# Optimization experiments

Measured on AMD Instinct MI355X. Metric: run time of the kernel, lower is better.

Reference implementation:

```python
import jax, jax.numpy as jnp
import numpy as np

N = 100000
E = 3200000
B = 8192
IN_DIM = 18   # enc_dim for khops=2
HID = 64
EMB = 32


def setup_inputs() -> dict:
    key = jax.random.key(0)
    ks = jax.random.split(key, 10)
    x = jax.random.normal(ks[0], (N, IN_DIM), dtype=jnp.float32)
    ei = jax.random.randint(ks[1], (2, E), 0, N, dtype=jnp.int64)
    targets = jax.random.randint(ks[2], (2, B), 0, N, dtype=jnp.int64)
    # GCN layer params (glorot-ish scale)
    W1 = jax.random.normal(ks[3], (IN_DIM, HID), dtype=jnp.float32) / np.sqrt(IN_DIM)
    b1 = jnp.zeros((HID,), dtype=jnp.float32)
    W2 = jax.random.normal(ks[4], (HID, EMB), dtype=jnp.float32) / np.sqrt(HID)
    b2 = jnp.zeros((EMB,), dtype=jnp.float32)
    Wo = jax.random.normal(ks[5], (EMB, 1), dtype=jnp.float32) / np.sqrt(EMB)
    bo = jnp.zeros((1,), dtype=jnp.float32)
    return {"x": x, "ei": ei, "targets": targets,
            "W1": W1, "b1": b1, "W2": W2, "b2": b2, "Wo": Wo, "bo": bo}


def _gcn_conv(x, W, b, src, dst, norm, n_nodes):
    # x' = D^{-1/2}(A+I)D^{-1/2} X W + b  (self-loops already in src/dst)
    h = x @ W                                  # [N, F_out]
    msg = h[src] * norm[:, None]               # [E+N, F_out] gather
    agg = jax.ops.segment_sum(msg, dst, num_segments=n_nodes)  # scatter-add
    return agg + b


def reference(x, ei, targets, W1, b1, W2, b2, Wo, bo):
    n = x.shape[0]
    loop = jnp.arange(n, dtype=ei.dtype)
    src = jnp.concatenate([ei[0], loop])
    dst = jnp.concatenate([ei[1], loop])
    deg = jax.ops.segment_sum(jnp.ones_like(src, dtype=x.dtype), dst, num_segments=n)
    dis = jax.lax.rsqrt(deg)                   # deg >= 1 (self-loops)
    norm = dis[src] * dis[dst]
    # 2-layer GCN (khops=2): relu between layers, dropout=0 (eval)
    h = jax.nn.relu(_gcn_conv(x, W1, b1, src, dst, norm, n))
    z = _gcn_conv(h, W2, b2, src, dst, norm, n)
    # node-pair multiply + linear head
    pair = z[targets[0]] * z[targets[1]]       # [B, EMB]
    return pair @ Wo + bo                      # [B, 1]
```

## Files before the change

kernel.cpp:

```cpp
#include <hip/hip_runtime.h>

#define IN_DIM 18
#define XPAD 20
#define HID 64
#define EMB 32
#define NGROUP 8
#define PSHIFT 9
#define PMAX 200
#define BCAP 80
#define TILE 4096
#define SCAP 16896
#define NPB 16

typedef int vint4 __attribute__((ext_vector_type(4)));
typedef unsigned int u32;

__device__ inline float4 shfl_f4(float4 v, int srcLane) {
    float4 r;
    r.x = __shfl(v.x, srcLane);
    r.y = __shfl(v.y, srcLane);
    r.z = __shfl(v.z, srcLane);
    r.w = __shfl(v.w, srcLane);
    return r;
}

__device__ inline float4 shfl_xor_f4(float4 v, int m) {
    v.x = __shfl_xor(v.x, m);
    v.y = __shfl_xor(v.y, m);
    v.z = __shfl_xor(v.z, m);
    v.w = __shfl_xor(v.w, m);
    return v;
}


__global__ void k_init(int* __restrict__ deg, int* __restrict__ gcnt, int n) {
    int i = blockIdx.x * 256 + threadIdx.x;
    if (i < n) deg[i] = 1;
    if (i < 256) gcnt[i] = 0;
}


__global__ void k_part(const int* __restrict__ src, const int* __restrict__ dst,
                       int* __restrict__ gcnt, u32* __restrict__ gbuf,
                       int e, int Pp, int cap) {
    __shared__ u32 sbuf[PMAX][BCAP];
    __shared__ int scnt[PMAX];
    __shared__ int sbase[PMAX];
    int tid = threadIdx.x;
    int ntile = (e + TILE - 1) / TILE;
    for (int tile = blockIdx.x; tile < ntile; tile += gridDim.x) {
        for (int p = tid; p < Pp; p += 256) scnt[p] = 0;
        __syncthreads();
#pragma unroll
        for (int r = 0; r < TILE / 1024; ++r) {
            int i = tile * TILE + (r * 256 + tid) * 4;
            if (i + 4 <= e) {
                vint4 s4 = __builtin_nontemporal_load((const vint4*)(src + i));
                vint4 d4 = __builtin_nontemporal_load((const vint4*)(dst + i));
#pragma unroll
                for (int k = 0; k < 4; ++k) {
                    int d = d4[k];
                    int p = d >> PSHIFT;
                    u32 pr = ((u32)s4[k] << PSHIFT) | (u32)(d & 511);
                    int pos = atomicAdd(&scnt[p], 1);
                    if (pos < BCAP) sbuf[p][pos] = pr;
                    else {
                        int gp = atomicAdd(&gcnt[p], 1);
                        __builtin_nontemporal_store(pr, &gbuf[(size_t)p * cap + gp]);
                    }
                }
            } else if (i < e) {
                for (int k = i; k < e; ++k) {
                    int d = dst[k];
                    int p = d >> PSHIFT;
                    u32 pr = ((u32)src[k] << PSHIFT) | (u32)(d & 511);
                    int pos = atomicAdd(&scnt[p], 1);
                    if (pos < BCAP) sbuf[p][pos] = pr;
                    else {
                        int gp = atomicAdd(&gcnt[p], 1);
                        __builtin_nontemporal_store(pr, &gbuf[(size_t)p * cap + gp]);
                    }
                }
            }
        }
        __syncthreads();
        for (int p = tid; p < Pp; p += 256)
            sbase[p] = atomicAdd(&gcnt[p], min(scnt[p], BCAP));
        __syncthreads();
        int wid = tid >> 6, lane = tid & 63;
        for (int p = wid; p < Pp; p += 4) {
            int c = min(scnt[p], BCAP);
            int b = sbase[p];
            for (int k = lane; k < c; k += 64)
                __builtin_nontemporal_store(sbuf[p][k], &gbuf[(size_t)p * cap + b + k]);
        }
        __syncthreads();
    }
}


__global__ void k_gscan(const int* __restrict__ gcnt, int* __restrict__ gbase, int Pp) {
    __shared__ int s[256];
    int t = threadIdx.x;
    int v = (t < Pp) ? gcnt[t] : 0;
    s[t] = v;
    __syncthreads();
    for (int off = 1; off < 256; off <<= 1) {
        int u = (t >= off) ? s[t - off] : 0;
        __syncthreads();
        s[t] += u;
        __syncthreads();
    }
    if (t < Pp) gbase[t] = s[t] - v;
}


__global__ void k_build(const u32* __restrict__ gbuf, const int* __restrict__ gcnt,
                        const int* __restrict__ gbase, int* __restrict__ deg,
                        float* __restrict__ dis, int* __restrict__ row_ptr,
                        int* __restrict__ adj, int cap, int n) {
    __shared__ u32 spairs[SCAP];
    __shared__ int sdeg[512];
    __shared__ int sexcl[512];
    __shared__ int swp[512];
    __shared__ int sscan[512];
    int p = blockIdx.x;
    int tid = threadIdx.x;
    int lo = p << PSHIFT;
    int nn = min(n - lo, 512);
    int cnt = gcnt[p];
    int base = gbase[p];
    const u32* buf = gbuf + (size_t)p * cap;

    sdeg[tid] = 0;
    int scap = min(cnt, SCAP);
    for (int k = tid; k < scap; k += 512)
        spairs[k] = __builtin_nontemporal_load(&buf[k]);
    __syncthreads();
    for (int k = tid; k < cnt; k += 512) {
        u32 pr = (k < SCAP) ? spairs[k] : __builtin_nontemporal_load(&buf[k]);
        atomicAdd(&sdeg[pr & 511], 1);
    }
    __syncthreads();
    int v = sdeg[tid];
    sscan[tid] = v;
    __syncthreads();
    for (int off = 1; off < 512; off <<= 1) {
        int u = (tid >= off) ? sscan[tid - off] : 0;
        __syncthreads();
        sscan[tid] += u;
        __syncthreads();
    }
    sexcl[tid] = sscan[tid] - v;
    swp[tid] = 0;
    __syncthreads();
    if (tid < nn) {
        int dg = sdeg[tid] + 1;
        deg[lo + tid] = dg;
        dis[lo + tid] = rsqrtf((float)dg);
        row_ptr[lo + tid] = base + sexcl[tid];
    }
    for (int k = tid; k < cnt; k += 512) {
        u32 pr = (k < SCAP) ? spairs[k] : __builtin_nontemporal_load(&buf[k]);
        int dl = pr & 511;
        int slot = sexcl[dl] + atomicAdd(&swp[dl], 1);
        adj[base + slot] = (int)(pr >> PSHIFT);
    }
}


__global__ void k_count_part(const int* __restrict__ dst, int* __restrict__ deg,
                             int e, int nrange, int n) {
    int g  = blockIdx.x & (NGROUP - 1);
    int lo = g * nrange;
    int hi = min(n, lo + nrange);
    int bid  = blockIdx.x >> 3;
    int nblk = gridDim.x >> 3;
    int i0   = (bid * 256 + threadIdx.x) * 4;
    int step = nblk * 256 * 4;
    for (int i = i0; i < e; i += step) {
        if (i + 4 <= e) {
            int4 d4 = *(const int4*)(dst + i);
            if (d4.x >= lo && d4.x < hi) atomicAdd(&deg[d4.x], 1);
            if (d4.y >= lo && d4.y < hi) atomicAdd(&deg[d4.y], 1);
            if (d4.z >= lo && d4.z < hi) atomicAdd(&deg[d4.z], 1);
            if (d4.w >= lo && d4.w < hi) atomicAdd(&deg[d4.w], 1);
        } else {
            for (int k = i; k < e; ++k) {
                int d = dst[k];
                if (d >= lo && d < hi) atomicAdd(&deg[d], 1);
            }
        }
    }
}

__global__ void k_dis(const int* __restrict__ deg, float* __restrict__ dis, int n) {
    int i = blockIdx.x * 256 + threadIdx.x;
    if (i < n) dis[i] = rsqrtf((float)deg[i]);
}

__global__ void k_scanA(const int* __restrict__ deg, int* __restrict__ row_ptr,
                        int* __restrict__ blksums, int n) {
    __shared__ int s[1024];
    int tid = threadIdx.x;
    int i = blockIdx.x * 1024 + tid;
    int v = (i < n) ? (deg[i] - 1) : 0;
    s[tid] = v;
    __syncthreads();
    for (int off = 1; off < 1024; off <<= 1) {
        int t = (tid >= off) ? s[tid - off] : 0;
        __syncthreads();
        s[tid] += t;
        __syncthreads();
    }
    if (i < n) row_ptr[i] = s[tid] - v;
    if (tid == 1023) blksums[blockIdx.x] = s[1023];
}

__global__ void k_scanB(const int* __restrict__ blksums, int* __restrict__ blkoffs, int nb) {
    __shared__ int s[1024];
    int tid = threadIdx.x;
    int v = (tid < nb) ? blksums[tid] : 0;
    s[tid] = v;
    __syncthreads();
    for (int off = 1; off < 1024; off <<= 1) {
        int t = (tid >= off) ? s[tid - off] : 0;
        __syncthreads();
        s[tid] += t;
        __syncthreads();
    }
    if (tid < nb) blkoffs[tid] = s[tid] - v;
}

__global__ void k_scanC(int* __restrict__ row_ptr, const int* __restrict__ blkoffs,
                        int* __restrict__ write_ptr, int n) {
    int i = blockIdx.x * 1024 + threadIdx.x;
    if (i < n) {
        int r = row_ptr[i] + blkoffs[blockIdx.x];
        row_ptr[i] = r;
        write_ptr[i] = r;
    }
}

__global__ void k_fill_part(const int* __restrict__ src, const int* __restrict__ dst,
                            int* __restrict__ write_ptr, int* __restrict__ adj,
                            int e, int nrange, int n) {
    int g  = blockIdx.x & (NGROUP - 1);
    int lo = g * nrange;
    int hi = min(n, lo + nrange);
    int bid  = blockIdx.x >> 3;
    int nblk = gridDim.x >> 3;
    int i0   = (bid * 256 + threadIdx.x) * 4;
    int step = nblk * 256 * 4;
    for (int i = i0; i < e; i += step) {
        if (i + 4 <= e) {
            int4 d4 = *(const int4*)(dst + i);
            if (d4.x >= lo && d4.x < hi) { int slot = atomicAdd(&write_ptr[d4.x], 1); adj[slot] = src[i];     }
            if (d4.y >= lo && d4.y < hi) { int slot = atomicAdd(&write_ptr[d4.y], 1); adj[slot] = src[i + 1]; }
            if (d4.z >= lo && d4.z < hi) { int slot = atomicAdd(&write_ptr[d4.z], 1); adj[slot] = src[i + 2]; }
            if (d4.w >= lo && d4.w < hi) { int slot = atomicAdd(&write_ptr[d4.w], 1); adj[slot] = src[i + 3]; }
        } else {
            for (int k = i; k < e; ++k) {
                int d = dst[k];
                if (d >= lo && d < hi) { int slot = atomicAdd(&write_ptr[d], 1); adj[slot] = src[k]; }
            }
        }
    }
}


__global__ void k_xn(const float* __restrict__ x, const float* __restrict__ dis,
                     float* __restrict__ xn, int n) {
    int gid = blockIdx.x * 256 + threadIdx.x;
    if (gid >= n * 5) return;
    int i = gid / 5, s = gid - (gid / 5) * 5;
    float dn = dis[i];
    const float* xr = x + (size_t)i * IN_DIM;
    float4 v;
    int k = s * 4;
    v.x = (k + 0 < IN_DIM) ? xr[k + 0] * dn : 0.f;
    v.y = (k + 1 < IN_DIM) ? xr[k + 1] * dn : 0.f;
    v.z = (k + 2 < IN_DIM) ? xr[k + 2] * dn : 0.f;
    v.w = (k + 3 < IN_DIM) ? xr[k + 3] * dn : 0.f;
    *(float4*)(xn + (size_t)i * XPAD + k) = v;
}


__global__ void k_agg1f(const float* __restrict__ xn, const int* __restrict__ row_ptr,
                        const int* __restrict__ deg, const int* __restrict__ adj,
                        const float* __restrict__ dis, const float* __restrict__ W1,
                        const float* __restrict__ b1, const float* __restrict__ W2,
                        float* __restrict__ hn2, int n) {
    __shared__ float sw[IN_DIM * HID];
    __shared__ float sw2[HID * EMB];
    __shared__ float sb[HID];
    __shared__ __align__(16) float sagg[4][XPAD];
    __shared__ float sh[4][HID];
    int tid = threadIdx.x;
    for (int t = tid; t < IN_DIM * HID; t += 256) sw[t] = W1[t];
    for (int t = tid; t < HID * EMB; t += 256) sw2[t] = W2[t];
    if (tid < HID) sb[tid] = b1[tid];
    __syncthreads();
    int lane = tid & 63;
    int wv = tid >> 6;
    int eg = lane / 5;
    int sl = lane - eg * 5;
    bool act = eg < 12;

    for (int nd = wv; nd < NPB; nd += 4) {
        int node = blockIdx.x * NPB + nd;
        if (node >= n) break;
        int beg = row_ptr[node];
        int cnt = deg[node] - 1;
        const int* a = adj + beg;
        float4 acc = make_float4(0.f, 0.f, 0.f, 0.f);
        int base = 0;
        for (; base + 24 <= cnt; base += 24) {
            if (act) {
                int j0 = a[base + eg];
                int j1 = a[base + 12 + eg];
                float4 v0 = *(const float4*)(xn + (size_t)j0 * XPAD + sl * 4);
                float4 v1 = *(const float4*)(xn + (size_t)j1 * XPAD + sl * 4);
                acc.x += v0.x + v1.x; acc.y += v0.y + v1.y;
                acc.z += v0.z + v1.z; acc.w += v0.w + v1.w;
            }
        }
        if (act && base + eg < cnt) {
            float4 v = *(const float4*)(xn + (size_t)a[base + eg] * XPAD + sl * 4);
            acc.x += v.x; acc.y += v.y; acc.z += v.z; acc.w += v.w;
        }
        if (act && base + 12 + eg < cnt) {
            float4 v = *(const float4*)(xn + (size_t)a[base + 12 + eg] * XPAD + sl * 4);
            acc.x += v.x; acc.y += v.y; acc.z += v.z; acc.w += v.w;
        }
        float4 t = shfl_f4(acc, lane + 30);
        if (lane < 30) { acc.x += t.x; acc.y += t.y; acc.z += t.z; acc.w += t.w; }
        t = shfl_f4(acc, lane + 15);
        if (lane < 15) { acc.x += t.x; acc.y += t.y; acc.z += t.z; acc.w += t.w; }
        t = shfl_f4(acc, lane + 10);
        if (lane < 5) { acc.x += t.x; acc.y += t.y; acc.z += t.z; acc.w += t.w; }
        t = shfl_f4(acc, lane + 5);
        if (lane < 5) { acc.x += t.x; acc.y += t.y; acc.z += t.z; acc.w += t.w; }
        float dn = dis[node];
        if (lane < 5) {
            float4 s4v = *(const float4*)(xn + (size_t)node * XPAD + lane * 4);
            acc.x += s4v.x; acc.y += s4v.y; acc.z += s4v.z; acc.w += s4v.w;
            *(float4*)&sagg[wv][lane * 4] = acc;
        }
        float s = 0.f;
#pragma unroll
        for (int k = 0; k < IN_DIM; ++k) s += sagg[wv][k] * sw[k * HID + lane];
        float hv = dn * s + sb[lane];
        sh[wv][lane] = hv > 0.f ? hv : 0.f;
        int g = lane & 31, half = lane >> 5;
        float s2 = 0.f;
#pragma unroll
        for (int k = 0; k < 32; ++k)
            s2 += sh[wv][half * 32 + k] * sw2[(half * 32 + k) * EMB + g];
        s2 += __shfl_xor(s2, 32);
        if (half == 0) hn2[(size_t)node * EMB + g] = dn * s2;
    }
}


__global__ void k_agg2(const float* __restrict__ hn2, const int* __restrict__ row_ptr,
                       const int* __restrict__ deg, const int* __restrict__ adj,
                       const float* __restrict__ dis, const float* __restrict__ b2,
                       float* __restrict__ z, int n) {
    int node = blockIdx.x * 4 + (threadIdx.x >> 6);
    if (node >= n) return;
    int lane = threadIdx.x & 63;
    int eg = lane >> 3;
    int d4 = lane & 7;
    int beg = row_ptr[node];
    int cnt = deg[node] - 1;
    const int* a = adj + beg;
    float4 acc = make_float4(0.f, 0.f, 0.f, 0.f);
    int base = 0;
    for (; base + 24 <= cnt; base += 24) {
        int j0 = a[base + eg];
        int j1 = a[base + 8 + eg];
        int j2 = a[base + 16 + eg];
        float4 v0 = *(const float4*)(hn2 + (size_t)j0 * EMB + d4 * 4);
        float4 v1 = *(const float4*)(hn2 + (size_t)j1 * EMB + d4 * 4);
        float4 v2 = *(const float4*)(hn2 + (size_t)j2 * EMB + d4 * 4);
        acc.x += v0.x + v1.x + v2.x; acc.y += v0.y + v1.y + v2.y;
        acc.z += v0.z + v1.z + v2.z; acc.w += v0.w + v1.w + v2.w;
    }
    int kk = base + eg;
    if (kk < cnt) {
        float4 v = *(const float4*)(hn2 + (size_t)a[kk] * EMB + d4 * 4);
        acc.x += v.x; acc.y += v.y; acc.z += v.z; acc.w += v.w;
    }
    kk += 8;
    if (kk < cnt) {
        float4 v = *(const float4*)(hn2 + (size_t)a[kk] * EMB + d4 * 4);
        acc.x += v.x; acc.y += v.y; acc.z += v.z; acc.w += v.w;
    }
    kk += 8;
    if (kk < cnt) {
        float4 v = *(const float4*)(hn2 + (size_t)a[kk] * EMB + d4 * 4);
        acc.x += v.x; acc.y += v.y; acc.z += v.z; acc.w += v.w;
    }
    float4 t = shfl_xor_f4(acc, 8);
    acc.x += t.x; acc.y += t.y; acc.z += t.z; acc.w += t.w;
    t = shfl_xor_f4(acc, 16);
    acc.x += t.x; acc.y += t.y; acc.z += t.z; acc.w += t.w;
    t = shfl_xor_f4(acc, 32);
    acc.x += t.x; acc.y += t.y; acc.z += t.z; acc.w += t.w;
    if (eg == 0) {
        float4 self = *(const float4*)(hn2 + (size_t)node * EMB + d4 * 4);
        float4 bb = *(const float4*)(b2 + d4 * 4);
        float dn = dis[node];
        float4 o;
        o.x = dn * (acc.x + self.x) + bb.x;
        o.y = dn * (acc.y + self.y) + bb.y;
        o.z = dn * (acc.z + self.z) + bb.z;
        o.w = dn * (acc.w + self.w) + bb.w;
        *(float4*)(z + (size_t)node * EMB + d4 * 4) = o;
    }
}


__global__ void k_head(const float* __restrict__ z, const int* __restrict__ tg,
                       const float* __restrict__ Wo, const float* __restrict__ bo,
                       float* __restrict__ out, int btot) {
    int i = blockIdx.x * 256 + threadIdx.x;
    if (i >= btot) return;
    int t0 = tg[i], t1 = tg[btot + i];
    const float* z0 = z + (size_t)t0 * EMB;
    const float* z1 = z + (size_t)t1 * EMB;
    float acc = 0.f;
#pragma unroll
    for (int g = 0; g < EMB; ++g) acc += z0[g] * z1[g] * Wo[g];
    out[i] = acc + bo[0];
}


extern "C" void kernel_launch(void* const* d_in, const int* in_sizes, int n_in,
                              void* d_out, int out_size, void* d_ws, size_t ws_size,
                              hipStream_t stream) {
    const float* x  = (const float*)d_in[0];
    const int*   ei = (const int*)d_in[1];
    const int*   tg = (const int*)d_in[2];
    const float* W1 = (const float*)d_in[3];
    const float* b1 = (const float*)d_in[4];
    const float* W2 = (const float*)d_in[5];
    const float* b2 = (const float*)d_in[6];
    const float* Wo = (const float*)d_in[7];
    const float* bo = (const float*)d_in[8];
    float* out = (float*)d_out;

    int n = in_sizes[0] / IN_DIM;
    int e = in_sizes[1] / 2;
    int b = in_sizes[2] / 2;
    const int* src = ei;
    const int* dst = ei + e;

    char* ws = (char*)d_ws;
    size_t off = 0;
    auto alloc = [&](size_t bytes) -> char* {
        char* p = ws + off;
        off += (bytes + 255) & ~(size_t)255;
        return p;
    };
    int*   deg       = (int*)alloc((size_t)n * 4);
    int*   row_ptr   = (int*)alloc((size_t)n * 4);
    int*   write_ptr = (int*)alloc((size_t)n * 4);
    int*   blksums   = (int*)alloc(1024 * 4);
    int*   blkoffs   = (int*)alloc(1024 * 4);
    float* dis       = (float*)alloc((size_t)n * 4);
    int*   adj       = (int*)alloc((size_t)e * 4);
    float* xn        = (float*)alloc((size_t)n * XPAD * 4);
    float* bufA      = (float*)alloc((size_t)n * EMB * 4);
    float* bufB      = (float*)alloc((size_t)n * EMB * 4);
    int*   gcnt      = (int*)alloc(1024);
    int*   gbase     = (int*)alloc(1024);

    int Pp = (n + 511) >> PSHIFT;
    int meanb = (Pp > 0) ? (e / Pp) : e;
    int cap = meanb + meanb / 16 + 1024;
    size_t bucket_bytes = (size_t)Pp * cap * 4;
    bool use_buckets = (Pp <= PMAX) && (n < (1 << 23)) &&
                       ((off + bucket_bytes + 256) <= ws_size);
    u32* gbuf = (u32*)alloc(bucket_bytes);

    int nb1024 = (n + 1023) / 1024;
    int nrange = (n + NGROUP - 1) / NGROUP;

    k_init<<<(n + 255) / 256, 256, 0, stream>>>(deg, gcnt, n);

    if (use_buckets) {
        k_part<<<512, 256, 0, stream>>>(src, dst, gcnt, gbuf, e, Pp, cap);
        k_gscan<<<1, 256, 0, stream>>>(gcnt, gbase, Pp);
        k_build<<<Pp, 512, 0, stream>>>(gbuf, gcnt, gbase, deg, dis, row_ptr, adj, cap, n);
    } else {
        k_count_part<<<2048, 256, 0, stream>>>(dst, deg, e, nrange, n);
        k_dis<<<(n + 255) / 256, 256, 0, stream>>>(deg, dis, n);
        k_scanA<<<nb1024, 1024, 0, stream>>>(deg, row_ptr, blksums, n);
        k_scanB<<<1, 1024, 0, stream>>>(blksums, blkoffs, nb1024);
        k_scanC<<<nb1024, 1024, 0, stream>>>(row_ptr, blkoffs, write_ptr, n);
        k_fill_part<<<2048, 256, 0, stream>>>(src, dst, write_ptr, adj, e, nrange, n);
    }

    k_xn<<<((size_t)n * 5 + 255) / 256, 256, 0, stream>>>(x, dis, xn, n);
    k_agg1f<<<(n + NPB - 1) / NPB, 256, 0, stream>>>(xn, row_ptr, deg, adj, dis, W1, b1, W2, bufA, n);
    k_agg2<<<(n + 3) / 4, 256, 0, stream>>>(bufA, row_ptr, deg, adj, dis, b2, bufB, n);

    k_head<<<(b + 255) / 256, 256, 0, stream>>>(bufB, tg, Wo, bo, out, b);
}
```

Measured before the change: 233.3 us.

## Split layer-1 feature gather into column slices with separate SpMM passes

The padded 20-float normalized input rows are split into three column-sliced arrays (8, 8 and 4 floats), and the first-layer neighbor aggregation runs as three separate SpMM kernels, each gathering a narrow slice with full-wave lane use. Each slice's working set is smaller and more cache-resident, and lanes are no longer idle under the old 12x5 mapping. The dense W1/ReLU/W2 transform moves to its own kernel that reads the aggregated rows. The cost is reading the adjacency list three times, extra kernel launches, and a round trip of the aggregate through global memory.

```diff
diff --git a/kernel.cpp b/kernel.cpp
--- a/kernel.cpp
+++ b/kernel.cpp
@@ -14,15 +14,6 @@
 
 typedef int vint4 __attribute__((ext_vector_type(4)));
 typedef unsigned int u32;
-
-__device__ inline float4 shfl_f4(float4 v, int srcLane) {
-    float4 r;
-    r.x = __shfl(v.x, srcLane);
-    r.y = __shfl(v.y, srcLane);
-    r.z = __shfl(v.z, srcLane);
-    r.w = __shfl(v.w, srcLane);
-    return r;
-}
 
 __device__ inline float4 shfl_xor_f4(float4 v, int m) {
     v.x = __shfl_xor(v.x, m);
@@ -270,7 +261,8 @@
 
 
 __global__ void k_xn(const float* __restrict__ x, const float* __restrict__ dis,
-                     float* __restrict__ xn, int n) {
+                     float* __restrict__ xs0, float* __restrict__ xs1,
+                     float* __restrict__ xs2, int n) {
     int gid = blockIdx.x * 256 + threadIdx.x;
     if (gid >= n * 5) return;
     int i = gid / 5, s = gid - (gid / 5) * 5;
@@ -282,15 +274,105 @@
     v.y = (k + 1 < IN_DIM) ? xr[k + 1] * dn : 0.f;
     v.z = (k + 2 < IN_DIM) ? xr[k + 2] * dn : 0.f;
     v.w = (k + 3 < IN_DIM) ? xr[k + 3] * dn : 0.f;
-    *(float4*)(xn + (size_t)i * XPAD + k) = v;
-}
-
-
-__global__ void k_agg1f(const float* __restrict__ xn, const int* __restrict__ row_ptr,
-                        const int* __restrict__ deg, const int* __restrict__ adj,
-                        const float* __restrict__ dis, const float* __restrict__ W1,
-                        const float* __restrict__ b1, const float* __restrict__ W2,
-                        float* __restrict__ hn2, int n) {
+    if (s < 2)      *(float4*)(xs0 + (size_t)i * 8 + s * 4) = v;
+    else if (s < 4) *(float4*)(xs1 + (size_t)i * 8 + (s - 2) * 4) = v;
+    else            *(float4*)(xs2 + (size_t)i * 4) = v;
+}
+
+
+__global__ void k_sp2s(const float* __restrict__ xs, const int* __restrict__ row_ptr,
+                       const int* __restrict__ deg, const int* __restrict__ adj,
+                       float* __restrict__ agg, int aggoff, int n) {
+    int node = blockIdx.x * 4 + (threadIdx.x >> 6);
+    if (node >= n) return;
+    int lane = threadIdx.x & 63;
+    int eg = lane >> 1, sl = lane & 1;
+    int beg = row_ptr[node];
+    int cnt = deg[node] - 1;
+    const int* a = adj + beg;
+    float4 acc = make_float4(0.f, 0.f, 0.f, 0.f);
+    int base = 0;
+    for (; base + 64 <= cnt; base += 64) {
+        int j0 = __builtin_nontemporal_load(&a[base + eg]);
+        int j1 = __builtin_nontemporal_load(&a[base + 32 + eg]);
+        float4 v0 = *(const float4*)(xs + (size_t)j0 * 8 + sl * 4);
+        float4 v1 = *(const float4*)(xs + (size_t)j1 * 8 + sl * 4);
+        acc.x += v0.x + v1.x; acc.y += v0.y + v1.y;
+        acc.z += v0.z + v1.z; acc.w += v0.w + v1.w;
+    }
+    if (base + eg < cnt) {
+        int j = __builtin_nontemporal_load(&a[base + eg]);
+        float4 v = *(const float4*)(xs + (size_t)j * 8 + sl * 4);
+        acc.x += v.x; acc.y += v.y; acc.z += v.z; acc.w += v.w;
+    }
+    if (base + 32 + eg < cnt) {
+        int j = __builtin_nontemporal_load(&a[base + 32 + eg]);
+        float4 v = *(const float4*)(xs + (size_t)j * 8 + sl * 4);
+        acc.x += v.x; acc.y += v.y; acc.z += v.z; acc.w += v.w;
+    }
+    float4 t = shfl_xor_f4(acc, 2);  acc.x += t.x; acc.y += t.y; acc.z += t.z; acc.w += t.w;
+    t = shfl_xor_f4(acc, 4);  acc.x += t.x; acc.y += t.y; acc.z += t.z; acc.w += t.w;
+    t = shfl_xor_f4(acc, 8);  acc.x += t.x; acc.y += t.y; acc.z += t.z; acc.w += t.w;
+    t = shfl_xor_f4(acc, 16); acc.x += t.x; acc.y += t.y; acc.z += t.z; acc.w += t.w;
+    t = shfl_xor_f4(acc, 32); acc.x += t.x; acc.y += t.y; acc.z += t.z; acc.w += t.w;
+    if (lane < 2) {
+        float4 self = *(const float4*)(xs + (size_t)node * 8 + lane * 4);
+        acc.x += self.x; acc.y += self.y; acc.z += self.z; acc.w += self.w;
+        __builtin_nontemporal_store(acc.x, agg + (size_t)node * XPAD + aggoff + lane * 4 + 0);
+        __builtin_nontemporal_store(acc.y, agg + (size_t)node * XPAD + aggoff + lane * 4 + 1);
+        __builtin_nontemporal_store(acc.z, agg + (size_t)node * XPAD + aggoff + lane * 4 + 2);
+        __builtin_nontemporal_store(acc.w, agg + (size_t)node * XPAD + aggoff + lane * 4 + 3);
+    }
+}
+
+
+__global__ void k_sp1s(const float* __restrict__ xs, const int* __restrict__ row_ptr,
+                       const int* __restrict__ deg, const int* __restrict__ adj,
+                       float* __restrict__ agg, int aggoff, int n) {
+    int node = blockIdx.x * 4 + (threadIdx.x >> 6);
+    if (node >= n) return;
+    int lane = threadIdx.x & 63;
+    int beg = row_ptr[node];
+    int cnt = deg[node] - 1;
+    const int* a = adj + beg;
+    float4 acc = make_float4(0.f, 0.f, 0.f, 0.f);
+    int base = 0;
+    for (; base + 128 <= cnt; base += 128) {
+        int j0 = __builtin_nontemporal_load(&a[base + lane]);
+        int j1 = __builtin_nontemporal_load(&a[base + 64 + lane]);
+        float4 v0 = *(const float4*)(xs + (size_t)j0 * 4);
+        float4 v1 = *(const float4*)(xs + (size_t)j1 * 4);
+        acc.x += v0.x + v1.x; acc.y += v0.y + v1.y;
+        acc.z += v0.z + v1.z; acc.w += v0.w + v1.w;
+    }
+    if (base + lane < cnt) {
+        int j = __builtin_nontemporal_load(&a[base + lane]);
+        float4 v = *(const float4*)(xs + (size_t)j * 4);
+        acc.x += v.x; acc.y += v.y; acc.z += v.z; acc.w += v.w;
+    }
+    if (base + 64 + lane < cnt) {
+        int j = __builtin_nontemporal_load(&a[base + 64 + lane]);
+        float4 v = *(const float4*)(xs + (size_t)j * 4);
+        acc.x += v.x; acc.y += v.y; acc.z += v.z; acc.w += v.w;
+    }
+    for (int m = 1; m <= 32; m <<= 1) {
+        float4 t = shfl_xor_f4(acc, m);
+        acc.x += t.x; acc.y += t.y; acc.z += t.z; acc.w += t.w;
+    }
+    if (lane == 0) {
+        float4 self = *(const float4*)(xs + (size_t)node * 4);
+        acc.x += self.x; acc.y += self.y; acc.z += self.z; acc.w += self.w;
+        __builtin_nontemporal_store(acc.x, agg + (size_t)node * XPAD + aggoff + 0);
+        __builtin_nontemporal_store(acc.y, agg + (size_t)node * XPAD + aggoff + 1);
+        __builtin_nontemporal_store(acc.z, agg + (size_t)node * XPAD + aggoff + 2);
+        __builtin_nontemporal_store(acc.w, agg + (size_t)node * XPAD + aggoff + 3);
+    }
+}
+
+
+__global__ void k_w12(const float* __restrict__ agg, const float* __restrict__ dis,
+                      const float* __restrict__ W1, const float* __restrict__ b1,
+                      const float* __restrict__ W2, float* __restrict__ hn2, int n) {
     __shared__ float sw[IN_DIM * HID];
     __shared__ float sw2[HID * EMB];
     __shared__ float sb[HID];
@@ -303,49 +385,13 @@
     __syncthreads();
     int lane = tid & 63;
     int wv = tid >> 6;
-    int eg = lane / 5;
-    int sl = lane - eg * 5;
-    bool act = eg < 12;
-
     for (int nd = wv; nd < NPB; nd += 4) {
         int node = blockIdx.x * NPB + nd;
         if (node >= n) break;
-        int beg = row_ptr[node];
-        int cnt = deg[node] - 1;
-        const int* a = adj + beg;
-        float4 acc = make_float4(0.f, 0.f, 0.f, 0.f);
-        int base = 0;
-        for (; base + 24 <= cnt; base += 24) {
-            if (act) {
-                int j0 = a[base + eg];
-                int j1 = a[base + 12 + eg];
-                float4 v0 = *(const float4*)(xn + (size_t)j0 * XPAD + sl * 4);
-                float4 v1 = *(const float4*)(xn + (size_t)j1 * XPAD + sl * 4);
-                acc.x += v0.x + v1.x; acc.y += v0.y + v1.y;
-                acc.z += v0.z + v1.z; acc.w += v0.w + v1.w;
-            }
-        }
-        if (act && base + eg < cnt) {
-            float4 v = *(const float4*)(xn + (size_t)a[base + eg] * XPAD + sl * 4);
-            acc.x += v.x; acc.y += v.y; acc.z += v.z; acc.w += v.w;
-        }
-        if (act && base + 12 + eg < cnt) {
-            float4 v = *(const float4*)(xn + (size_t)a[base + 12 + eg] * XPAD + sl * 4);
-            acc.x += v.x; acc.y += v.y; acc.z += v.z; acc.w += v.w;
-        }
-        float4 t = shfl_f4(acc, lane + 30);
-        if (lane < 30) { acc.x += t.x; acc.y += t.y; acc.z += t.z; acc.w += t.w; }
-        t = shfl_f4(acc, lane + 15);
-        if (lane < 15) { acc.x += t.x; acc.y += t.y; acc.z += t.z; acc.w += t.w; }
-        t = shfl_f4(acc, lane + 10);
-        if (lane < 5) { acc.x += t.x; acc.y += t.y; acc.z += t.z; acc.w += t.w; }
-        t = shfl_f4(acc, lane + 5);
-        if (lane < 5) { acc.x += t.x; acc.y += t.y; acc.z += t.z; acc.w += t.w; }
         float dn = dis[node];
         if (lane < 5) {
-            float4 s4v = *(const float4*)(xn + (size_t)node * XPAD + lane * 4);
-            acc.x += s4v.x; acc.y += s4v.y; acc.z += s4v.z; acc.w += s4v.w;
-            *(float4*)&sagg[wv][lane * 4] = acc;
+            float4 v = *(const float4*)(agg + (size_t)node * XPAD + lane * 4);
+            *(float4*)&sagg[wv][lane * 4] = v;
         }
         float s = 0.f;
 #pragma unroll
@@ -471,7 +517,10 @@
     int*   blkoffs   = (int*)alloc(1024 * 4);
     float* dis       = (float*)alloc((size_t)n * 4);
     int*   adj       = (int*)alloc((size_t)e * 4);
-    float* xn        = (float*)alloc((size_t)n * XPAD * 4);
+    float* xs0       = (float*)alloc((size_t)n * 8 * 4);
+    float* xs1       = (float*)alloc((size_t)n * 8 * 4);
+    float* xs2       = (float*)alloc((size_t)n * 4 * 4);
+    float* agg       = (float*)alloc((size_t)n * XPAD * 4);
     float* bufA      = (float*)alloc((size_t)n * EMB * 4);
     float* bufB      = (float*)alloc((size_t)n * EMB * 4);
     int*   gcnt      = (int*)alloc(1024);
@@ -487,6 +536,7 @@
 
     int nb1024 = (n + 1023) / 1024;
     int nrange = (n + NGROUP - 1) / NGROUP;
+    int nblk4 = (n + 3) / 4;
 
     k_init<<<(n + 255) / 256, 256, 0, stream>>>(deg, gcnt, n);
 
@@ -503,9 +553,14 @@
         k_fill_part<<<2048, 256, 0, stream>>>(src, dst, write_ptr, adj, e, nrange, n);
     }
 
-    k_xn<<<((size_t)n * 5 + 255) / 256, 256, 0, stream>>>(x, dis, xn, n);
-    k_agg1f<<<(n + NPB - 1) / NPB, 256, 0, stream>>>(xn, row_ptr, deg, adj, dis, W1, b1, W2, bufA, n);
-    k_agg2<<<(n + 3) / 4, 256, 0, stream>>>(bufA, row_ptr, deg, adj, dis, b2, bufB, n);
+    k_xn<<<((size_t)n * 5 + 255) / 256, 256, 0, stream>>>(x, dis, xs0, xs1, xs2, n);
+
+    k_sp2s<<<nblk4, 256, 0, stream>>>(xs0, row_ptr, deg, adj, agg, 0, n);
+    k_sp2s<<<nblk4, 256, 0, stream>>>(xs1, row_ptr, deg, adj, agg, 8, n);
+    k_sp1s<<<nblk4, 256, 0, stream>>>(xs2, row_ptr, deg, adj, agg, 16, n);
+    k_w12<<<(n + NPB - 1) / NPB, 256, 0, stream>>>(agg, dis, W1, b1, W2, bufA, n);
+
+    k_agg2<<<nblk4, 256, 0, stream>>>(bufA, row_ptr, deg, adj, dis, b2, bufB, n);
 
     k_head<<<(b + 255) / 256, 256, 0, stream>>>(bufB, tg, Wo, bo, out, b);
 }
```

After: 299.1 us. 28.2% more time.

## Fold bucket scan into build, drop init launch, split layer-2 GEMM out of agg1

Applied to the files above, without the earlier changes.

Removes the separate global scan kernel by having each k_build block recompute the prefix over bucket counts in shared memory. In the bucket path, the full-size degree init kernel is replaced by a one-block zero of the counters. k_agg1f now handles one node per wave, with no W2 staged in shared memory, and writes the 64-wide hidden layer to a new buffer. A separate k_gemm2 kernel then applies W2. This should cut shared-memory use and raise occupancy in the aggregation kernel, and it removes small launches. In exchange it adds an extra round trip of the N×64 hidden tensor through global memory plus one more launch.

```diff
diff --git a/kernel.cpp b/kernel.cpp
--- a/kernel.cpp
+++ b/kernel.cpp
@@ -10,7 +10,6 @@
 #define BCAP 80
 #define TILE 4096
 #define SCAP 16896
-#define NPB 16
 
 typedef int vint4 __attribute__((ext_vector_type(4)));
 typedef unsigned int u32;
@@ -32,6 +31,10 @@
     return v;
 }
 
+
+__global__ void k_zero(int* __restrict__ gcnt) {
+    gcnt[threadIdx.x] = 0;
+}
 
 __global__ void k_init(int* __restrict__ deg, int* __restrict__ gcnt, int n) {
     int i = blockIdx.x * 256 + threadIdx.x;
@@ -99,26 +102,10 @@
 }
 
 
-__global__ void k_gscan(const int* __restrict__ gcnt, int* __restrict__ gbase, int Pp) {
-    __shared__ int s[256];
-    int t = threadIdx.x;
-    int v = (t < Pp) ? gcnt[t] : 0;
-    s[t] = v;
-    __syncthreads();
-    for (int off = 1; off < 256; off <<= 1) {
-        int u = (t >= off) ? s[t - off] : 0;
-        __syncthreads();
-        s[t] += u;
-        __syncthreads();
-    }
-    if (t < Pp) gbase[t] = s[t] - v;
-}
-
-
 __global__ void k_build(const u32* __restrict__ gbuf, const int* __restrict__ gcnt,
-                        const int* __restrict__ gbase, int* __restrict__ deg,
-                        float* __restrict__ dis, int* __restrict__ row_ptr,
-                        int* __restrict__ adj, int cap, int n) {
+                        int* __restrict__ deg, float* __restrict__ dis,
+                        int* __restrict__ row_ptr, int* __restrict__ adj,
+                        int cap, int n, int Pp) {
     __shared__ u32 spairs[SCAP];
     __shared__ int sdeg[512];
     __shared__ int sexcl[512];
@@ -129,8 +116,19 @@
     int lo = p << PSHIFT;
     int nn = min(n - lo, 512);
     int cnt = gcnt[p];
-    int base = gbase[p];
     const u32* buf = gbuf + (size_t)p * cap;
+
+    if (tid < 256) sscan[tid] = (tid < Pp) ? gcnt[tid] : 0;
+    __syncthreads();
+    for (int off = 1; off < 256; off <<= 1) {
+        int u = 0;
+        if (tid < 256 && tid >= off) u = sscan[tid - off];
+        __syncthreads();
+        if (tid < 256) sscan[tid] += u;
+        __syncthreads();
+    }
+    int base = sscan[p] - cnt;
+    __syncthreads();
 
     sdeg[tid] = 0;
     int scap = min(cnt, SCAP);
@@ -289,77 +287,78 @@
 __global__ void k_agg1f(const float* __restrict__ xn, const int* __restrict__ row_ptr,
                         const int* __restrict__ deg, const int* __restrict__ adj,
                         const float* __restrict__ dis, const float* __restrict__ W1,
-                        const float* __restrict__ b1, const float* __restrict__ W2,
-                        float* __restrict__ hn2, int n) {
+                        const float* __restrict__ b1, float* __restrict__ h, int n) {
     __shared__ float sw[IN_DIM * HID];
-    __shared__ float sw2[HID * EMB];
     __shared__ float sb[HID];
     __shared__ __align__(16) float sagg[4][XPAD];
-    __shared__ float sh[4][HID];
     int tid = threadIdx.x;
     for (int t = tid; t < IN_DIM * HID; t += 256) sw[t] = W1[t];
-    for (int t = tid; t < HID * EMB; t += 256) sw2[t] = W2[t];
     if (tid < HID) sb[tid] = b1[tid];
     __syncthreads();
+    int node = blockIdx.x * 4 + (tid >> 6);
+    if (node >= n) return;
     int lane = tid & 63;
     int wv = tid >> 6;
     int eg = lane / 5;
     int sl = lane - eg * 5;
     bool act = eg < 12;
-
-    for (int nd = wv; nd < NPB; nd += 4) {
-        int node = blockIdx.x * NPB + nd;
-        if (node >= n) break;
-        int beg = row_ptr[node];
-        int cnt = deg[node] - 1;
-        const int* a = adj + beg;
-        float4 acc = make_float4(0.f, 0.f, 0.f, 0.f);
-        int base = 0;
-        for (; base + 24 <= cnt; base += 24) {
-            if (act) {
-                int j0 = a[base + eg];
-                int j1 = a[base + 12 + eg];
-                float4 v0 = *(const float4*)(xn + (size_t)j0 * XPAD + sl * 4);
-                float4 v1 = *(const float4*)(xn + (size_t)j1 * XPAD + sl * 4);
-                acc.x += v0.x + v1.x; acc.y += v0.y + v1.y;
-                acc.z += v0.z + v1.z; acc.w += v0.w + v1.w;
-            }
+    int beg = row_ptr[node];
+    int cnt = deg[node] - 1;
+    const int* a = adj + beg;
+    float4 acc = make_float4(0.f, 0.f, 0.f, 0.f);
+    int base = 0;
+    for (; base + 24 <= cnt; base += 24) {
+        if (act) {
+            int j0 = a[base + eg];
+            int j1 = a[base + 12 + eg];
+            float4 v0 = *(const float4*)(xn + (size_t)j0 * XPAD + sl * 4);
+            float4 v1 = *(const float4*)(xn + (size_t)j1 * XPAD + sl * 4);
+            acc.x += v0.x + v1.x; acc.y += v0.y + v1.y;
+            acc.z += v0.z + v1.z; acc.w += v0.w + v1.w;
         }
-        if (act && base + eg < cnt) {
-            float4 v = *(const float4*)(xn + (size_t)a[base + eg] * XPAD + sl * 4);
-            acc.x += v.x; acc.y += v.y; acc.z += v.z; acc.w += v.w;
-        }
-        if (act && base + 12 + eg < cnt) {
-            float4 v = *(const float4*)(xn + (size_t)a[base + 12 + eg] * XPAD + sl * 4);
-            acc.x += v.x; acc.y += v.y; acc.z += v.z; acc.w += v.w;
-        }
-        float4 t = shfl_f4(acc, lane + 30);
-        if (lane < 30) { acc.x += t.x; acc.y += t.y; acc.z += t.z; acc.w += t.w; }
-        t = shfl_f4(acc, lane + 15);
-        if (lane < 15) { acc.x += t.x; acc.y += t.y; acc.z += t.z; acc.w += t.w; }
-        t = shfl_f4(acc, lane + 10);
-        if (lane < 5) { acc.x += t.x; acc.y += t.y; acc.z += t.z; acc.w += t.w; }
-        t = shfl_f4(acc, lane + 5);
-        if (lane < 5) { acc.x += t.x; acc.y += t.y; acc.z += t.z; acc.w += t.w; }
-        float dn = dis[node];
-        if (lane < 5) {
-            float4 s4v = *(const float4*)(xn + (size_t)node * XPAD + lane * 4);
-            acc.x += s4v.x; acc.y += s4v.y; acc.z += s4v.z; acc.w += s4v.w;
-            *(float4*)&sagg[wv][lane * 4] = acc;
-        }
-        float s = 0.f;
+    }
+    if (act && base + eg < cnt) {
+        float4 v = *(const float4*)(xn + (size_t)a[base + eg] * XPAD + sl * 4);
+        acc.x += v.x; acc.y += v.y; acc.z += v.z; acc.w += v.w;
+    }
+    if (act && base + 12 + eg < cnt) {
+        float4 v = *(const float4*)(xn + (size_t)a[base + 12 + eg] * XPAD + sl * 4);
+        acc.x += v.x; acc.y += v.y; acc.z += v.z; acc.w += v.w;
+    }
+    float4 t = shfl_f4(acc, lane + 30);
+    if (lane < 30) { acc.x += t.x; acc.y += t.y; acc.z += t.z; acc.w += t.w; }
+    t = shfl_f4(acc, lane + 15);
+    if (lane < 15) { acc.x += t.x; acc.y += t.y; acc.z += t.z; acc.w += t.w; }
+    t = shfl_f4(acc, lane + 10);
+    if (lane < 5) { acc.x += t.x; acc.y += t.y; acc.z += t.z; acc.w += t.w; }
+    t = shfl_f4(acc, lane + 5);
+    if (lane < 5) { acc.x += t.x; acc.y += t.y; acc.z += t.z; acc.w += t.w; }
+    if (lane < 5) {
+        float4 s4v = *(const float4*)(xn + (size_t)node * XPAD + lane * 4);
+        acc.x += s4v.x; acc.y += s4v.y; acc.z += s4v.z; acc.w += s4v.w;
+        *(float4*)&sagg[wv][lane * 4] = acc;
+    }
+    float s = 0.f;
 #pragma unroll
-        for (int k = 0; k < IN_DIM; ++k) s += sagg[wv][k] * sw[k * HID + lane];
-        float hv = dn * s + sb[lane];
-        sh[wv][lane] = hv > 0.f ? hv : 0.f;
-        int g = lane & 31, half = lane >> 5;
-        float s2 = 0.f;
+    for (int k = 0; k < IN_DIM; ++k) s += sagg[wv][k] * sw[k * HID + lane];
+    float hv = dis[node] * s + sb[lane];
+    h[(size_t)node * HID + lane] = hv > 0.f ? hv : 0.f;
+}
+
+
+__global__ void k_gemm2(const float* __restrict__ h, const float* __restrict__ W2,
+                        const float* __restrict__ dis, float* __restrict__ hn2, int n) {
+    __shared__ float w[HID * EMB];
+    for (int t = threadIdx.x; t < HID * EMB; t += 256) w[t] = W2[t];
+    __syncthreads();
+    int gid = blockIdx.x * 256 + threadIdx.x;
+    int i = gid >> 5, g = gid & 31;
+    if (i >= n) return;
+    const float* hr = h + (size_t)i * HID;
+    float acc = 0.f;
 #pragma unroll
-        for (int k = 0; k < 32; ++k)
-            s2 += sh[wv][half * 32 + k] * sw2[(half * 32 + k) * EMB + g];
-        s2 += __shfl_xor(s2, 32);
-        if (half == 0) hn2[(size_t)node * EMB + g] = dn * s2;
-    }
+    for (int k = 0; k < HID; ++k) acc += hr[k] * w[k * EMB + g];
+    hn2[(size_t)i * EMB + g] = acc * dis[i];
 }
 
 
@@ -472,10 +471,10 @@
     float* dis       = (float*)alloc((size_t)n * 4);
     int*   adj       = (int*)alloc((size_t)e * 4);
     float* xn        = (float*)alloc((size_t)n * XPAD * 4);
+    float* bufH      = (float*)alloc((size_t)n * HID * 4);
     float* bufA      = (float*)alloc((size_t)n * EMB * 4);
     float* bufB      = (float*)alloc((size_t)n * EMB * 4);
     int*   gcnt      = (int*)alloc(1024);
-    int*   gbase     = (int*)alloc(1024);
 
     int Pp = (n + 511) >> PSHIFT;
     int meanb = (Pp > 0) ? (e / Pp) : e;
@@ -487,14 +486,14 @@
 
     int nb1024 = (n + 1023) / 1024;
     int nrange = (n + NGROUP - 1) / NGROUP;
-
-    k_init<<<(n + 255) / 256, 256, 0, stream>>>(deg, gcnt, n);
+    int nblk4 = (n + 3) / 4;
 
     if (use_buckets) {
+        k_zero<<<1, 256, 0, stream>>>(gcnt);
         k_part<<<512, 256, 0, stream>>>(src, dst, gcnt, gbuf, e, Pp, cap);
-        k_gscan<<<1, 256, 0, stream>>>(gcnt, gbase, Pp);
-        k_build<<<Pp, 512, 0, stream>>>(gbuf, gcnt, gbase, deg, dis, row_ptr, adj, cap, n);
+        k_build<<<Pp, 512, 0, stream>>>(gbuf, gcnt, deg, dis, row_ptr, adj, cap, n, Pp);
     } else {
+        k_init<<<(n + 255) / 256, 256, 0, stream>>>(deg, gcnt, n);
         k_count_part<<<2048, 256, 0, stream>>>(dst, deg, e, nrange, n);
         k_dis<<<(n + 255) / 256, 256, 0, stream>>>(deg, dis, n);
         k_scanA<<<nb1024, 1024, 0, stream>>>(deg, row_ptr, blksums, n);
@@ -504,8 +503,9 @@
     }
 
     k_xn<<<((size_t)n * 5 + 255) / 256, 256, 0, stream>>>(x, dis, xn, n);
-    k_agg1f<<<(n + NPB - 1) / NPB, 256, 0, stream>>>(xn, row_ptr, deg, adj, dis, W1, b1, W2, bufA, n);
-    k_agg2<<<(n + 3) / 4, 256, 0, stream>>>(bufA, row_ptr, deg, adj, dis, b2, bufB, n);
+    k_agg1f<<<nblk4, 256, 0, stream>>>(xn, row_ptr, deg, adj, dis, W1, b1, bufH, n);
+    k_gemm2<<<((size_t)n * EMB + 255) / 256, 256, 0, stream>>>(bufH, W2, dis, bufA, n);
+    k_agg2<<<nblk4, 256, 0, stream>>>(bufA, row_ptr, deg, adj, dis, b2, bufB, n);
 
     k_head<<<(b + 255) / 256, 256, 0, stream>>>(bufB, tg, Wo, bo, out, b);
 }
```

Measured after the change: 251.2 us. 7.7% more time.
